# Performance work log

Hardware: AMD Instinct MI355X
Metric: run time of the kernel (lower is better)

## Reference

```python
import jax, jax.numpy as jnp
import numpy as np

N_NODES = 50000
N_EDGES = 800000
N_FEAT = 100
HIDDEN = 100
N_CLASSES = 2
N_GRAPHS = 256


def setup_inputs() -> dict:
    key = jax.random.key(0)
    ks = jax.random.split(key, 16)
    x = jax.random.normal(ks[0], (N_NODES, N_FEAT), dtype=jnp.float32)
    edge_index = jax.random.randint(ks[1], (2, N_EDGES), 0, N_NODES, dtype=jnp.int64)
    batch = jnp.sort(jax.random.randint(ks[2], (N_NODES,), 0, N_GRAPHS, dtype=jnp.int64))
    def lin(k, fan_in, fan_out):
        s = 1.0 / np.sqrt(fan_in)
        return jax.random.uniform(k, (fan_in, fan_out), jnp.float32, -s, s)
    return {
        "x": x, "edge_index": edge_index, "batch": batch,
        # SAGEConv1: lin_l (neighbor aggr, with bias), lin_r (root, no bias)
        "W1l": lin(ks[3], N_FEAT, HIDDEN), "b1": jnp.zeros((HIDDEN,), jnp.float32), "W1r": lin(ks[4], N_FEAT, HIDDEN),
        "W2l": lin(ks[5], HIDDEN, HIDDEN), "b2": jnp.zeros((HIDDEN,), jnp.float32), "W2r": lin(ks[6], HIDDEN, HIDDEN),
        "W3l": lin(ks[7], HIDDEN, HIDDEN), "b3": jnp.zeros((HIDDEN,), jnp.float32), "W3r": lin(ks[8], HIDDEN, HIDDEN),
        "Wlin": lin(ks[9], HIDDEN, N_CLASSES), "blin": jnp.zeros((N_CLASSES,), jnp.float32),
    }


def _sage_conv(x, src, dst, Wl, b, Wr):
    # PyG SAGEConv with mean aggregation: out = lin_l(mean_{j in N(i)} x_j) + lin_r(x_i)
    msg = x[src]  # [E, d] gather
    s = jax.ops.segment_sum(msg, dst, num_segments=x.shape[0])  # [N, d]
    cnt = jax.ops.segment_sum(jnp.ones_like(dst, dtype=x.dtype), dst, num_segments=x.shape[0])
    aggr = s / jnp.maximum(cnt, 1.0)[:, None]
    return aggr @ Wl + b + x @ Wr


def reference(x, edge_index, batch, W1l, b1, W1r, W2l, b2, W2r, W3l, b3, W3r, Wlin, blin):
    src, dst = edge_index[0], edge_index[1]
    h = jax.nn.relu(_sage_conv(x, src, dst, W1l, b1, W1r))
    h = jax.nn.relu(_sage_conv(h, src, dst, W2l, b2, W2r))
    h = _sage_conv(h, src, dst, W3l, b3, W3r)
    # global_mean_pool over batch ids
    gs = jax.ops.segment_sum(h, batch, num_segments=N_GRAPHS)
    gc = jax.ops.segment_sum(jnp.ones_like(batch, dtype=h.dtype), batch, num_segments=N_GRAPHS)
    g = gs / jnp.maximum(gc, 1.0)[:, None]
    # dropout(p=0.5) is identity in eval mode
    return g @ Wlin + blin
```

## Files before the change

kernel.cpp:

```cpp
#include <hip/hip_runtime.h>
#include <hip/hip_bf16.h>

typedef __attribute__((ext_vector_type(8))) short short8v;
typedef __attribute__((ext_vector_type(4))) float f32x4;

#define PST 128
#define PSTL 136
#define MAXBUCK 1024

static __device__ inline unsigned short f2bf(float x) {
    union { float f; unsigned int u; } c; c.f = x;
    unsigned int r = (c.u + 0x7FFFu + ((c.u >> 16) & 1u)) >> 16;
    return (unsigned short)r;
}
static __device__ inline float bf2f(unsigned short h) {
    union { float f; unsigned int u; } c; c.u = ((unsigned int)h) << 16;
    return c.f;
}
static __device__ inline f32x4 MF(short8v a, short8v b, f32x4 c) {
    return __builtin_amdgcn_mfma_f32_16x16x32_bf16(a, b, c, 0, 0, 0);
}


__global__ __launch_bounds__(256) void k_bincount(const int* __restrict__ dst,
                                                  int* __restrict__ bcnt,
                                                  int n, int nbuck, int chunk) {
    __shared__ int lcnt[MAXBUCK];
    int t = threadIdx.x;
    for (int b = t; b < nbuck; b += 256) lcnt[b] = 0;
    __syncthreads();
    int e0 = blockIdx.x * chunk;
    int e1 = e0 + chunk; if (e1 > n) e1 = n;
    for (int e = e0 + t; e < e1; e += 256) atomicAdd(&lcnt[dst[e] >> 8], 1);
    __syncthreads();
    for (int b = t; b < nbuck; b += 256)
        if (lcnt[b]) atomicAdd(&bcnt[b], lcnt[b]);
}

__global__ __launch_bounds__(1024) void k_binscan(const int* __restrict__ bcnt,
                                                  int* __restrict__ bbase,
                                                  int* __restrict__ bcur,
                                                  int* __restrict__ rowp,
                                                  int nbuck, int n_nodes, int n_edges) {
    __shared__ int tmp[1024];
    int t = threadIdx.x;
    int v = (t < nbuck) ? bcnt[t] : 0;
    tmp[t] = v;
    __syncthreads();
    for (int off = 1; off < 1024; off <<= 1) {
        int u = 0;
        if (t >= off) u = tmp[t - off];
        __syncthreads();
        if (t >= off) tmp[t] += u;
        __syncthreads();
    }
    if (t < nbuck) { int b = tmp[t] - v; bbase[t] = b; bcur[t] = b; }
    if (t == 0) rowp[n_nodes] = n_edges;
}

__global__ __launch_bounds__(256) void k_binscatter(const int* __restrict__ src,
                                                    const int* __restrict__ dst,
                                                    int* __restrict__ bcur,
                                                    int2* __restrict__ tmpv,
                                                    int n, int nbuck, int chunk) {
    __shared__ int lcnt[MAXBUCK];
    __shared__ int lbase[MAXBUCK];
    int t = threadIdx.x;
    for (int b = t; b < nbuck; b += 256) lcnt[b] = 0;
    __syncthreads();
    int e0 = blockIdx.x * chunk;
    int e1 = e0 + chunk; if (e1 > n) e1 = n;
    for (int e = e0 + t; e < e1; e += 256) atomicAdd(&lcnt[dst[e] >> 8], 1);
    __syncthreads();
    for (int b = t; b < nbuck; b += 256) {
        int c = lcnt[b];
        lbase[b] = c ? atomicAdd(&bcur[b], c) : 0;
        lcnt[b] = 0;
    }
    __syncthreads();
    for (int e = e0 + t; e < e1; e += 256) {
        int d = dst[e];
        int b = d >> 8;
        int r = atomicAdd(&lcnt[b], 1);
        tmpv[lbase[b] + r] = make_int2(src[e], d);
    }
}

__global__ __launch_bounds__(256) void k_build(const int2* __restrict__ tmpv,
                                               const int* __restrict__ bbase,
                                               int* __restrict__ rowp,
                                               float* __restrict__ inv,
                                               int* __restrict__ ssrc,
                                               int n_nodes, int n_edges, int nbuck) {
    __shared__ int hist[256];
    __shared__ int scan[256];
    __shared__ int curs[256];
    int b = blockIdx.x;
    int t = threadIdx.x;
    int s = bbase[b];
    int e = (b + 1 < nbuck) ? bbase[b + 1] : n_edges;
    hist[t] = 0;
    __syncthreads();
    for (int i = s + t; i < e; i += 256) atomicAdd(&hist[tmpv[i].y & 255], 1);
    __syncthreads();
    int v = hist[t];
    scan[t] = v;
    __syncthreads();
    for (int off = 1; off < 256; off <<= 1) {
        int u = 0;
        if (t >= off) u = scan[t - off];
        __syncthreads();
        if (t >= off) scan[t] += u;
        __syncthreads();
    }
    int excl = scan[t] - v;
    curs[t] = excl;
    int node = (b << 8) + t;
    if (node < n_nodes) {
        rowp[node] = s + excl;
        inv[node] = 1.0f / (float)(v > 1 ? v : 1);
    }
    __syncthreads();
    for (int i = s + t; i < e; i += 256) {
        int2 p = tmpv[i];
        int r = atomicAdd(&curs[p.y & 255], 1);
        ssrc[s + r] = p.x;
    }
}

__global__ __launch_bounds__(256) void k_cvt(const float* __restrict__ X,
                                             unsigned short* __restrict__ Xhi,
                                             unsigned short* __restrict__ Xlo,
                                             int n) {
    int grp = threadIdx.x >> 4, l = threadIdx.x & 15;
    int i = blockIdx.x * 16 + grp;
    if (i >= n) return;
    unsigned short* ph = Xhi + (size_t)i * PST + l * 8;
    unsigned short* pl = Xlo + (size_t)i * PST + l * 8;
    if (l < 13) {
        float4 v0 = *(const float4*)(X + (size_t)i * 100 + l * 8);
        float4 v1 = (l < 12) ? *(const float4*)(X + (size_t)i * 100 + l * 8 + 4)
                             : make_float4(0.f, 0.f, 0.f, 0.f);
        float f[8] = {v0.x, v0.y, v0.z, v0.w, v1.x, v1.y, v1.z, v1.w};
        short8v hv, lv;
#pragma unroll
        for (int m = 0; m < 8; ++m) {
            unsigned short h = f2bf(f[m]);
            hv[m] = (short)h;
            lv[m] = (short)f2bf(f[m] - bf2f(h));
        }
        *(short8v*)ph = hv;
        *(short8v*)pl = lv;
    } else {
        short8v z = (short8v){0,0,0,0,0,0,0,0};
        *(short8v*)ph = z;
        *(short8v*)pl = z;
    }
}

#define PACKN (2 * 4 * 7 * 64)
__global__ __launch_bounds__(256) void k_pack3(const float* __restrict__ W1l, const float* __restrict__ W1r,
                                               const float* __restrict__ W2l, const float* __restrict__ W2r,
                                               const float* __restrict__ W3l, const float* __restrict__ W3r,
                                               unsigned short* __restrict__ B1h, unsigned short* __restrict__ B1l,
                                               unsigned short* __restrict__ B2h, unsigned short* __restrict__ B2l,
                                               unsigned short* __restrict__ B3h, unsigned short* __restrict__ B3l) {
    int gid = blockIdx.x * 256 + threadIdx.x;
    if (gid >= 3 * PACKN) return;
    int layer = gid / PACKN;
    int idx = gid - layer * PACKN;
    const float* Wl = layer == 0 ? W1l : (layer == 1 ? W2l : W3l);
    const float* Wr = layer == 0 ? W1r : (layer == 1 ? W2r : W3r);
    unsigned short* Bh = layer == 0 ? B1h : (layer == 1 ? B2h : B3h);
    unsigned short* Bl = layer == 0 ? B1l : (layer == 1 ? B2l : B3l);
    int lane = idx & 63;
    int t = idx >> 6;
    int nt = t % 7;
    int pc = t / 7;
    int part = pc >> 2, c = pc & 3;
    int col = nt * 16 + (lane & 15);
    int fbase = c * 32 + (lane >> 4) * 8;
    const float* W = part ? Wr : Wl;
    for (int jj = 0; jj < 8; ++jj) {
        int k = fbase + jj;
        float w = (k < 100 && col < 100) ? W[k * 100 + col] : 0.f;
        unsigned short h = f2bf(w);
        Bh[(size_t)idx * 8 + jj] = h;
        Bl[(size_t)idx * 8 + jj] = f2bf(w - bf2f(h));
    }
}

__global__ __launch_bounds__(128) void k_layer(const unsigned short* __restrict__ Xhi,
                                               const unsigned short* __restrict__ Xlo,
                                               const int* __restrict__ ssrc,
                                               const int* __restrict__ rowp,
                                               const float* __restrict__ inv,
                                               const unsigned short* __restrict__ Bh,
                                               const unsigned short* __restrict__ Bl,
                                               const float* __restrict__ bias,
                                               unsigned short* __restrict__ Ohi,
                                               unsigned short* __restrict__ Olo,
                                               int relu, int n) {
    __shared__ unsigned short lds_h[32][PSTL];
    __shared__ unsigned short lds_l[32][PSTL];
    const int t = threadIdx.x;
    const int base = blockIdx.x * 32;

    {
        const int grp = t >> 4, l = t & 15;
        const bool act = l < 13;
        const size_t loff = (size_t)l * 8;
        const short8v z = (short8v){0,0,0,0,0,0,0,0};
#pragma unroll
        for (int it = 0; it < 4; ++it) {
            const int lr = it * 8 + grp;
            const int node = base + lr;
            if (node < n) {
                int s = rowp[node];
                int e = rowp[node + 1];
                float a[8];
#pragma unroll
                for (int m = 0; m < 8; ++m) a[m] = 0.f;
                int i = s;
                for (; i + 4 <= e; i += 4) {
                    int s0 = ssrc[i], s1 = ssrc[i + 1], s2 = ssrc[i + 2], s3 = ssrc[i + 3];
                    if (act) {
                        short8v v0 = *(const short8v*)(Xhi + (size_t)s0 * PST + loff);
                        short8v v1 = *(const short8v*)(Xhi + (size_t)s1 * PST + loff);
                        short8v v2 = *(const short8v*)(Xhi + (size_t)s2 * PST + loff);
                        short8v v3 = *(const short8v*)(Xhi + (size_t)s3 * PST + loff);
#pragma unroll
                        for (int m = 0; m < 8; ++m)
                            a[m] += bf2f((unsigned short)v0[m]) + bf2f((unsigned short)v1[m])
                                  + bf2f((unsigned short)v2[m]) + bf2f((unsigned short)v3[m]);
                    }
                }
                for (; i < e; ++i) {
                    int s0 = ssrc[i];
                    if (act) {
                        short8v v0 = *(const short8v*)(Xhi + (size_t)s0 * PST + loff);
#pragma unroll
                        for (int m = 0; m < 8; ++m) a[m] += bf2f((unsigned short)v0[m]);
                    }
                }
                if (act) {
                    const float f = inv[node];
                    short8v hv, lv;
#pragma unroll
                    for (int m = 0; m < 8; ++m) {
                        float v = a[m] * f;
                        unsigned short h = f2bf(v);
                        hv[m] = (short)h;
                        lv[m] = (short)f2bf(v - bf2f(h));
                    }
                    *(short8v*)&lds_h[lr][l * 8] = hv;
                    *(short8v*)&lds_l[lr][l * 8] = lv;
                } else {
                    *(short8v*)&lds_h[lr][l * 8] = z;
                    *(short8v*)&lds_l[lr][l * 8] = z;
                }
            } else {
                *(short8v*)&lds_h[lr][l * 8] = z;
                *(short8v*)&lds_l[lr][l * 8] = z;
            }
        }
    }
    __syncthreads();

    const int lane = t & 63;
    const int wv = t >> 6;
    const int m0 = base + wv * 16;
    const int lrow = lane & 15;
    const int lg = lane >> 4;
    const int ldr = wv * 16 + lrow;

    f32x4 acc[7];
#pragma unroll
    for (int nt = 0; nt < 7; ++nt) acc[nt] = (f32x4){0.f, 0.f, 0.f, 0.f};

    int r0 = m0 + lrow; if (r0 >= n) r0 = n - 1;
    const size_t b0 = (size_t)r0 * PST + lg * 8;

#pragma unroll
    for (int c = 0; c < 4; ++c) {
        short8v ah0 = *(const short8v*)&lds_h[ldr][c * 32 + lg * 8];
        short8v al0 = *(const short8v*)&lds_l[ldr][c * 32 + lg * 8];
        const unsigned short* bph = Bh + ((size_t)(c * 7) * 64 + lane) * 8;
        const unsigned short* bpl = Bl + ((size_t)(c * 7) * 64 + lane) * 8;
#pragma unroll
        for (int nt = 0; nt < 7; ++nt) {
            short8v bh = *(const short8v*)(bph + nt * 512);
            short8v bl = *(const short8v*)(bpl + nt * 512);
            acc[nt] = MF(ah0, bh, acc[nt]);
            acc[nt] = MF(ah0, bl, acc[nt]);
            acc[nt] = MF(al0, bh, acc[nt]);
        }
    }
#pragma unroll
    for (int c = 0; c < 4; ++c) {
        short8v ah0 = *(const short8v*)(Xhi + b0 + c * 32);
        short8v al0 = *(const short8v*)(Xlo + b0 + c * 32);
        const unsigned short* bph = Bh + ((size_t)((4 + c) * 7) * 64 + lane) * 8;
        const unsigned short* bpl = Bl + ((size_t)((4 + c) * 7) * 64 + lane) * 8;
#pragma unroll
        for (int nt = 0; nt < 7; ++nt) {
            short8v bh = *(const short8v*)(bph + nt * 512);
            short8v bl = *(const short8v*)(bpl + nt * 512);
            acc[nt] = MF(ah0, bh, acc[nt]);
            acc[nt] = MF(ah0, bl, acc[nt]);
            acc[nt] = MF(al0, bh, acc[nt]);
        }
    }

#pragma unroll
    for (int nt = 0; nt < 7; ++nt) {
        int col = nt * 16 + lrow;
        bool cok = col < 100;
        float bb = cok ? bias[col] : 0.f;
#pragma unroll
        for (int r = 0; r < 4; ++r) {
            int row = m0 + lg * 4 + r;
            if (cok && row < n) {
                float v = acc[nt][r] + bb;
                if (relu) v = fmaxf(v, 0.f);
                unsigned short h = f2bf(v);
                size_t o = (size_t)row * PST + col;
                Ohi[o] = h;
                Olo[o] = f2bf(v - bf2f(h));
            }
        }
    }
    if (lane < 32) {
        int row = m0 + (lane >> 1);
        if (row < n) {
            unsigned short* op = ((lane & 1) == 0 ? Ohi : Olo) + (size_t)row * PST;
            short4 z4 = {0, 0, 0, 0};
            short8v z = (short8v){0,0,0,0,0,0,0,0};
            *(short4*)(op + 100) = z4;
            *(short8v*)(op + 104) = z;
            *(short8v*)(op + 112) = z;
            *(short8v*)(op + 120) = z;
        }
    }
}

__global__ __launch_bounds__(256) void k_pool(const unsigned short* __restrict__ Hhi,
                                              const unsigned short* __restrict__ Hlo,
                                              const int* __restrict__ batch,
                                              const float* __restrict__ Wlin,
                                              const float* __restrict__ blin,
                                              float* __restrict__ out, int n) {
    int g = blockIdx.x;
    int t = threadIdx.x;
    int grp = t >> 4, l = t & 15;
    int lo = 0, hi = n;
    while (lo < hi) { int m = (lo + hi) >> 1; if (batch[m] < g) lo = m + 1; else hi = m; }
    int lo2 = lo, hi2 = n;
    while (lo2 < hi2) { int m = (lo2 + hi2) >> 1; if (batch[m] < g + 1) lo2 = m + 1; else hi2 = m; }

    const bool act = l < 13;
    float a[8];
#pragma unroll
    for (int m = 0; m < 8; ++m) a[m] = 0.f;
    const size_t loff = (size_t)l * 8;
    for (int node = lo + grp; node < lo2; node += 16) {
        if (act) {
            short8v vh = *(const short8v*)(Hhi + (size_t)node * PST + loff);
            short8v vl = *(const short8v*)(Hlo + (size_t)node * PST + loff);
#pragma unroll
            for (int m = 0; m < 8; ++m)
                a[m] += bf2f((unsigned short)vh[m]) + bf2f((unsigned short)vl[m]);
        }
    }

    __shared__ float part[16][13][8];
    if (act) {
#pragma unroll
        for (int m = 0; m < 8; ++m) part[grp][l][m] = a[m];
    }
    __syncthreads();

    __shared__ float gm[104];
    if (t < 104) {
        int fg = t >> 3, m = t & 7;
        float s = 0.f;
#pragma unroll
        for (int q = 0; q < 16; ++q) s += part[q][fg][m];
        float f = (lo2 > lo) ? 1.0f / (float)(lo2 - lo) : 0.0f;
        gm[t] = s * f;
    }
    __syncthreads();
    if (t < 2) {
        float o = blin[t];
        for (int k = 0; k < 100; ++k) o += gm[k] * Wlin[k * 2 + t];
        out[g * 2 + t] = o;
    }
}


extern "C" void kernel_launch(void* const* d_in, const int* in_sizes, int n_in,
                              void* d_out, int out_size, void* d_ws, size_t ws_size,
                              hipStream_t stream) {
    const float* x    = (const float*)d_in[0];
    const int*   ei   = (const int*)d_in[1];
    const int*   batch= (const int*)d_in[2];
    const float* W1l  = (const float*)d_in[3];
    const float* b1   = (const float*)d_in[4];
    const float* W1r  = (const float*)d_in[5];
    const float* W2l  = (const float*)d_in[6];
    const float* b2   = (const float*)d_in[7];
    const float* W2r  = (const float*)d_in[8];
    const float* W3l  = (const float*)d_in[9];
    const float* b3   = (const float*)d_in[10];
    const float* W3r  = (const float*)d_in[11];
    const float* Wlin = (const float*)d_in[12];
    const float* blin = (const float*)d_in[13];
    float* out = (float*)d_out;

    const int n_nodes  = in_sizes[0] / 100;
    const int n_edges  = in_sizes[1] / 2;
    const int n_graphs = out_size / 2;
    const int* src = ei;
    const int* dst = ei + n_edges;

    char* ws = (char*)d_ws;
    size_t o = 0;
    auto alloc = [&](size_t bytes) { size_t r = o; o = (o + bytes + 255) & ~(size_t)255; return r; };
    int*   rowp = (int*)(ws + alloc((size_t)(n_nodes + 1) * 4));
    float* inv  = (float*)(ws + alloc((size_t)n_nodes * 4));
    int*   ssrc = (int*)(ws + alloc((size_t)n_edges * 4));
    int*   bcnt = (int*)(ws + alloc(MAXBUCK * 4));
    int*   bbase= (int*)(ws + alloc(MAXBUCK * 4));
    int*   bcur = (int*)(ws + alloc(MAXBUCK * 4));
    int2*  tmpv = (int2*)(ws + alloc((size_t)n_edges * 8));
    const size_t pbytes = (size_t)n_nodes * PST * 2;
    unsigned short* XAhi = (unsigned short*)(ws + alloc(pbytes));
    unsigned short* XAlo = (unsigned short*)(ws + alloc(pbytes));
    unsigned short* XBhi = (unsigned short*)(ws + alloc(pbytes));
    unsigned short* XBlo = (unsigned short*)(ws + alloc(pbytes));
    const size_t bfb = (size_t)PACKN * 8 * 2;
    unsigned short* B1h = (unsigned short*)(ws + alloc(bfb));
    unsigned short* B1l = (unsigned short*)(ws + alloc(bfb));
    unsigned short* B2h = (unsigned short*)(ws + alloc(bfb));
    unsigned short* B2l = (unsigned short*)(ws + alloc(bfb));
    unsigned short* B3h = (unsigned short*)(ws + alloc(bfb));
    unsigned short* B3l = (unsigned short*)(ws + alloc(bfb));

    hipMemsetAsync(bcnt, 0, MAXBUCK * 4, stream);

    const int nbuck = (n_nodes + 255) >> 8;
    const int chunk = (n_edges + 255) / 256;

    k_bincount<<<256, 256, 0, stream>>>(dst, bcnt, n_edges, nbuck, chunk);
    k_binscan<<<1, 1024, 0, stream>>>(bcnt, bbase, bcur, rowp, nbuck, n_nodes, n_edges);
    k_binscatter<<<256, 256, 0, stream>>>(src, dst, bcur, tmpv, n_edges, nbuck, chunk);
    k_build<<<nbuck, 256, 0, stream>>>(tmpv, bbase, rowp, inv, ssrc,
                                       n_nodes, n_edges, nbuck);

    k_pack3<<<(3 * PACKN + 255) / 256, 256, 0, stream>>>(
        W1l, W1r, W2l, W2r, W3l, W3r, B1h, B1l, B2h, B2l, B3h, B3l);

    const int nb16 = (n_nodes + 15) / 16;
    const int lgrid = (n_nodes + 31) / 32;

    k_cvt<<<nb16, 256, 0, stream>>>(x, XAhi, XAlo, n_nodes);

    k_layer<<<lgrid, 128, 0, stream>>>(XAhi, XAlo, ssrc, rowp, inv, B1h, B1l, b1,
                                       XBhi, XBlo, 1, n_nodes);
    k_layer<<<lgrid, 128, 0, stream>>>(XBhi, XBlo, ssrc, rowp, inv, B2h, B2l, b2,
                                       XAhi, XAlo, 1, n_nodes);
    k_layer<<<lgrid, 128, 0, stream>>>(XAhi, XAlo, ssrc, rowp, inv, B3h, B3l, b3,
                                       XBhi, XBlo, 0, n_nodes);

    k_pool<<<n_graphs, 256, 0, stream>>>(XBhi, XBlo, batch, Wlin, blin, out, n_nodes);
}
```

Measured before the change: 235.3 us.

## Aggregate neighbors directly into MFMA operand layout, dropping LDS staging

```diff
diff --git a/kernel.cpp b/kernel.cpp
--- a/kernel.cpp
+++ b/kernel.cpp
@@ -5,7 +5,6 @@
 typedef __attribute__((ext_vector_type(4))) float f32x4;
 
 #define PST 128
-#define PSTL 136
 #define MAXBUCK 1024
 
 static __device__ inline unsigned short f2bf(float x) {
@@ -190,125 +189,118 @@
     }
 }
 
-__global__ __launch_bounds__(128) void k_layer(const unsigned short* __restrict__ Xhi,
-                                               const unsigned short* __restrict__ Xlo,
-                                               const int* __restrict__ ssrc,
-                                               const int* __restrict__ rowp,
-                                               const float* __restrict__ inv,
-                                               const unsigned short* __restrict__ Bh,
-                                               const unsigned short* __restrict__ Bl,
-                                               const float* __restrict__ bias,
-                                               unsigned short* __restrict__ Ohi,
-                                               unsigned short* __restrict__ Olo,
-                                               int relu, int n) {
-    __shared__ unsigned short lds_h[32][PSTL];
-    __shared__ unsigned short lds_l[32][PSTL];
-    const int t = threadIdx.x;
-    const int base = blockIdx.x * 32;
-
-    {
-        const int grp = t >> 4, l = t & 15;
-        const bool act = l < 13;
-        const size_t loff = (size_t)l * 8;
-        const short8v z = (short8v){0,0,0,0,0,0,0,0};
-#pragma unroll
-        for (int it = 0; it < 4; ++it) {
-            const int lr = it * 8 + grp;
-            const int node = base + lr;
-            if (node < n) {
-                int s = rowp[node];
-                int e = rowp[node + 1];
-                float a[8];
-#pragma unroll
-                for (int m = 0; m < 8; ++m) a[m] = 0.f;
-                int i = s;
-                for (; i + 4 <= e; i += 4) {
-                    int s0 = ssrc[i], s1 = ssrc[i + 1], s2 = ssrc[i + 2], s3 = ssrc[i + 3];
-                    if (act) {
-                        short8v v0 = *(const short8v*)(Xhi + (size_t)s0 * PST + loff);
-                        short8v v1 = *(const short8v*)(Xhi + (size_t)s1 * PST + loff);
-                        short8v v2 = *(const short8v*)(Xhi + (size_t)s2 * PST + loff);
-                        short8v v3 = *(const short8v*)(Xhi + (size_t)s3 * PST + loff);
-#pragma unroll
-                        for (int m = 0; m < 8; ++m)
-                            a[m] += bf2f((unsigned short)v0[m]) + bf2f((unsigned short)v1[m])
-                                  + bf2f((unsigned short)v2[m]) + bf2f((unsigned short)v3[m]);
-                    }
-                }
-                for (; i < e; ++i) {
-                    int s0 = ssrc[i];
-                    if (act) {
-                        short8v v0 = *(const short8v*)(Xhi + (size_t)s0 * PST + loff);
-#pragma unroll
-                        for (int m = 0; m < 8; ++m) a[m] += bf2f((unsigned short)v0[m]);
-                    }
-                }
-                if (act) {
-                    const float f = inv[node];
-                    short8v hv, lv;
-#pragma unroll
-                    for (int m = 0; m < 8; ++m) {
-                        float v = a[m] * f;
-                        unsigned short h = f2bf(v);
-                        hv[m] = (short)h;
-                        lv[m] = (short)f2bf(v - bf2f(h));
-                    }
-                    *(short8v*)&lds_h[lr][l * 8] = hv;
-                    *(short8v*)&lds_l[lr][l * 8] = lv;
-                } else {
-                    *(short8v*)&lds_h[lr][l * 8] = z;
-                    *(short8v*)&lds_l[lr][l * 8] = z;
-                }
-            } else {
-                *(short8v*)&lds_h[lr][l * 8] = z;
-                *(short8v*)&lds_l[lr][l * 8] = z;
-            }
-        }
-    }
-    __syncthreads();
-
-    const int lane = t & 63;
-    const int wv = t >> 6;
-    const int m0 = base + wv * 16;
+__global__ __launch_bounds__(64) void k_layer(const unsigned short* __restrict__ Xhi,
+                                              const unsigned short* __restrict__ Xlo,
+                                              const int* __restrict__ ssrc,
+                                              const int* __restrict__ rowp,
+                                              const float* __restrict__ inv,
+                                              const unsigned short* __restrict__ Bh,
+                                              const unsigned short* __restrict__ Bl,
+                                              const float* __restrict__ bias,
+                                              unsigned short* __restrict__ Ohi,
+                                              unsigned short* __restrict__ Olo,
+                                              int relu, int n) {
+    const int lane = threadIdx.x;
     const int lrow = lane & 15;
     const int lg = lane >> 4;
-    const int ldr = wv * 16 + lrow;
+    const int m0 = blockIdx.x * 16;
+    const int node = m0 + lrow;
+
+    float am[4][8];
+#pragma unroll
+    for (int c = 0; c < 4; ++c)
+#pragma unroll
+        for (int m = 0; m < 8; ++m) am[c][m] = 0.f;
+
+    int s = 0, deg = 0;
+    float fin = 0.f;
+    if (node < n) {
+        s = rowp[node];
+        deg = rowp[node + 1] - s;
+        fin = inv[node];
+    }
+    const size_t coff = (size_t)lg * 8;
+
+    int i = 0;
+    for (; i + 2 <= deg; i += 2) {
+        int s0 = ssrc[s + i];
+        int s1 = ssrc[s + i + 1];
+        const unsigned short* r0 = Xhi + (size_t)s0 * PST + coff;
+        const unsigned short* r1 = Xhi + (size_t)s1 * PST + coff;
+        short8v v00 = *(const short8v*)(r0);
+        short8v v01 = *(const short8v*)(r0 + 32);
+        short8v v02 = *(const short8v*)(r0 + 64);
+        short8v v03 = *(const short8v*)(r0 + 96);
+        short8v v10 = *(const short8v*)(r1);
+        short8v v11 = *(const short8v*)(r1 + 32);
+        short8v v12 = *(const short8v*)(r1 + 64);
+        short8v v13 = *(const short8v*)(r1 + 96);
+#pragma unroll
+        for (int m = 0; m < 8; ++m) {
+            am[0][m] += bf2f((unsigned short)v00[m]) + bf2f((unsigned short)v10[m]);
+            am[1][m] += bf2f((unsigned short)v01[m]) + bf2f((unsigned short)v11[m]);
+            am[2][m] += bf2f((unsigned short)v02[m]) + bf2f((unsigned short)v12[m]);
+            am[3][m] += bf2f((unsigned short)v03[m]) + bf2f((unsigned short)v13[m]);
+        }
+    }
+    if (i < deg) {
+        int s0 = ssrc[s + i];
+        const unsigned short* r0 = Xhi + (size_t)s0 * PST + coff;
+        short8v v00 = *(const short8v*)(r0);
+        short8v v01 = *(const short8v*)(r0 + 32);
+        short8v v02 = *(const short8v*)(r0 + 64);
+        short8v v03 = *(const short8v*)(r0 + 96);
+#pragma unroll
+        for (int m = 0; m < 8; ++m) {
+            am[0][m] += bf2f((unsigned short)v00[m]);
+            am[1][m] += bf2f((unsigned short)v01[m]);
+            am[2][m] += bf2f((unsigned short)v02[m]);
+            am[3][m] += bf2f((unsigned short)v03[m]);
+        }
+    }
 
     f32x4 acc[7];
 #pragma unroll
     for (int nt = 0; nt < 7; ++nt) acc[nt] = (f32x4){0.f, 0.f, 0.f, 0.f};
 
-    int r0 = m0 + lrow; if (r0 >= n) r0 = n - 1;
-    const size_t b0 = (size_t)r0 * PST + lg * 8;
-
 #pragma unroll
     for (int c = 0; c < 4; ++c) {
-        short8v ah0 = *(const short8v*)&lds_h[ldr][c * 32 + lg * 8];
-        short8v al0 = *(const short8v*)&lds_l[ldr][c * 32 + lg * 8];
+        short8v ah, al;
+#pragma unroll
+        for (int m = 0; m < 8; ++m) {
+            float v = am[c][m] * fin;
+            unsigned short h = f2bf(v);
+            ah[m] = (short)h;
+            al[m] = (short)f2bf(v - bf2f(h));
+        }
         const unsigned short* bph = Bh + ((size_t)(c * 7) * 64 + lane) * 8;
         const unsigned short* bpl = Bl + ((size_t)(c * 7) * 64 + lane) * 8;
 #pragma unroll
         for (int nt = 0; nt < 7; ++nt) {
             short8v bh = *(const short8v*)(bph + nt * 512);
             short8v bl = *(const short8v*)(bpl + nt * 512);
-            acc[nt] = MF(ah0, bh, acc[nt]);
-            acc[nt] = MF(ah0, bl, acc[nt]);
-            acc[nt] = MF(al0, bh, acc[nt]);
-        }
-    }
-#pragma unroll
-    for (int c = 0; c < 4; ++c) {
-        short8v ah0 = *(const short8v*)(Xhi + b0 + c * 32);
-        short8v al0 = *(const short8v*)(Xlo + b0 + c * 32);
-        const unsigned short* bph = Bh + ((size_t)((4 + c) * 7) * 64 + lane) * 8;
-        const unsigned short* bpl = Bl + ((size_t)((4 + c) * 7) * 64 + lane) * 8;
-#pragma unroll
-        for (int nt = 0; nt < 7; ++nt) {
-            short8v bh = *(const short8v*)(bph + nt * 512);
-            short8v bl = *(const short8v*)(bpl + nt * 512);
-            acc[nt] = MF(ah0, bh, acc[nt]);
-            acc[nt] = MF(ah0, bl, acc[nt]);
-            acc[nt] = MF(al0, bh, acc[nt]);
+            acc[nt] = MF(ah, bh, acc[nt]);
+            acc[nt] = MF(ah, bl, acc[nt]);
+            acc[nt] = MF(al, bh, acc[nt]);
+        }
+    }
+    {
+        int r0i = node < n ? node : (n - 1);
+        const size_t b0 = (size_t)r0i * PST + coff;
+#pragma unroll
+        for (int c = 0; c < 4; ++c) {
+            short8v ah = *(const short8v*)(Xhi + b0 + c * 32);
+            short8v al = *(const short8v*)(Xlo + b0 + c * 32);
+            const unsigned short* bph = Bh + ((size_t)((4 + c) * 7) * 64 + lane) * 8;
+            const unsigned short* bpl = Bl + ((size_t)((4 + c) * 7) * 64 + lane) * 8;
+#pragma unroll
+            for (int nt = 0; nt < 7; ++nt) {
+                short8v bh = *(const short8v*)(bph + nt * 512);
+                short8v bl = *(const short8v*)(bpl + nt * 512);
+                acc[nt] = MF(ah, bh, acc[nt]);
+                acc[nt] = MF(ah, bl, acc[nt]);
+                acc[nt] = MF(al, bh, acc[nt]);
+            }
         }
     }
 
@@ -461,16 +453,16 @@
         W1l, W1r, W2l, W2r, W3l, W3r, B1h, B1l, B2h, B2l, B3h, B3l);
 
     const int nb16 = (n_nodes + 15) / 16;
-    const int lgrid = (n_nodes + 31) / 32;
+    const int lgrid = (n_nodes + 15) / 16;
 
     k_cvt<<<nb16, 256, 0, stream>>>(x, XAhi, XAlo, n_nodes);
 
-    k_layer<<<lgrid, 128, 0, stream>>>(XAhi, XAlo, ssrc, rowp, inv, B1h, B1l, b1,
-                                       XBhi, XBlo, 1, n_nodes);
-    k_layer<<<lgrid, 128, 0, stream>>>(XBhi, XBlo, ssrc, rowp, inv, B2h, B2l, b2,
-                                       XAhi, XAlo, 1, n_nodes);
-    k_layer<<<lgrid, 128, 0, stream>>>(XAhi, XAlo, ssrc, rowp, inv, B3h, B3l, b3,
-                                       XBhi, XBlo, 0, n_nodes);
+    k_layer<<<lgrid, 64, 0, stream>>>(XAhi, XAlo, ssrc, rowp, inv, B1h, B1l, b1,
+                                      XBhi, XBlo, 1, n_nodes);
+    k_layer<<<lgrid, 64, 0, stream>>>(XBhi, XBlo, ssrc, rowp, inv, B2h, B2l, b2,
+                                      XAhi, XAlo, 1, n_nodes);
+    k_layer<<<lgrid, 64, 0, stream>>>(XAhi, XAlo, ssrc, rowp, inv, B3h, B3l, b3,
+                                      XBhi, XBlo, 0, n_nodes);
 
     k_pool<<<n_graphs, 256, 0, stream>>>(XBhi, XBlo, batch, Wlin, blin, out, n_nodes);
 }
```

Result: slower. 269.8 us (+14.7%).
